# Optimization experiments

Measured on AMD Instinct MI355X. Metric: run time of the kernel, lower is better.

## Reference

```python
import jax, jax.numpy as jnp
import numpy as np

NEG_SLOPE = 0.2  # PyG GATConv default leaky_relu slope
N_NODES, N_EDGES, F_IN, HID = 25000, 200000, 64, 128


def gat_layer(x, src, dst, W, a_src, a_dst, b, heads, ch):
    """PyG-style GATConv (concat=True, eval mode). x:[N,Fin] -> [N,heads*ch]."""
    N = x.shape[0]
    h = (x @ W).reshape(N, heads, ch)                      # [N,H,C]
    al_s = jnp.sum(h * a_src, axis=-1)                     # [N,H]
    al_d = jnp.sum(h * a_dst, axis=-1)                     # [N,H]
    e = jax.nn.leaky_relu(al_s[src] + al_d[dst], NEG_SLOPE)  # [E,H]
    # segment softmax over incoming edges of each dst node (stable)
    e = e - jax.ops.segment_max(e, dst, num_segments=N)[dst]
    ex = jnp.exp(e)
    alpha = ex / jax.ops.segment_sum(ex, dst, num_segments=N)[dst]  # [E,H]
    out = jax.ops.segment_sum(h[src] * alpha[:, :, None], dst, num_segments=N)  # [N,H,C]
    return out.reshape(N, heads * ch) + b


def setup_inputs() -> dict:
    key = jax.random.key(0)
    ks = jax.random.split(key, 24)
    def g(k, shape, fan_in):
        return jax.random.normal(k, shape, dtype=jnp.float32) / np.sqrt(fan_in)
    inp = {
        "x": jax.random.normal(ks[0], (N_NODES, F_IN), dtype=jnp.float32),
        "edge_index": jax.random.randint(ks[1], (2, N_EDGES), 0, N_NODES, dtype=jnp.int64) if jax.config.jax_enable_x64 else jax.random.randint(ks[1], (2, N_EDGES), 0, N_NODES).astype(jnp.int32),
        "liquor_idx": jax.random.randint(ks[2], (4096,), 0, N_NODES),
        "ingredient_idx": jax.random.randint(ks[3], (4096,), 0, N_NODES),
        "W1": g(ks[4], (F_IN, 8 * HID), F_IN), "a_s1": g(ks[5], (8, HID), HID), "a_d1": g(ks[6], (8, HID), HID), "b1": jnp.zeros((8 * HID,), jnp.float32),
        "W2": g(ks[7], (8 * HID, 8 * HID), 8 * HID), "a_s2": g(ks[8], (8, HID), HID), "a_d2": g(ks[9], (8, HID), HID), "b2": jnp.zeros((8 * HID,), jnp.float32),
        "W3": g(ks[10], (8 * HID, HID), 8 * HID), "a_s3": g(ks[11], (1, HID), HID), "a_d3": g(ks[12], (1, HID), HID), "b3": jnp.zeros((HID,), jnp.float32),
        # MLP scorer: 256 -> 128 -> 64 -> 1
        "mw1": g(ks[13], (2 * HID, HID), 2 * HID), "mb1": jnp.zeros((HID,), jnp.float32),
        "mw2": g(ks[14], (HID, HID // 2), HID), "mb2": jnp.zeros((HID // 2,), jnp.float32),
        "mw3": g(ks[15], (HID // 2, 1), HID // 2), "mb3": jnp.zeros((1,), jnp.float32),
    }
    return inp


def reference(x, edge_index, liquor_idx, ingredient_idx,
              W1, a_s1, a_d1, b1, W2, a_s2, a_d2, b2, W3, a_s3, a_d3, b3,
              mw1, mb1, mw2, mb2, mw3, mb3):
    N = x.shape[0]
    loops = jnp.arange(N, dtype=edge_index.dtype)  # GATConv adds self-loops
    src = jnp.concatenate([edge_index[0], loops])
    dst = jnp.concatenate([edge_index[1], loops])
    h = jax.nn.relu(gat_layer(x, src, dst, W1, a_s1, a_d1, b1, 8, HID))
    h = jax.nn.relu(gat_layer(h, src, dst, W2, a_s2, a_d2, b2, 8, HID))
    h = gat_layer(h, src, dst, W3, a_s3, a_d3, b3, 1, HID)
    pair = jnp.concatenate([h[liquor_idx], h[ingredient_idx]], axis=-1)  # [B,256]
    z = jax.nn.relu(pair @ mw1 + mb1)
    z = jax.nn.relu(z @ mw2 + mb2)
    z = z @ mw3 + mb3
    return jax.nn.sigmoid(z).squeeze(-1)
```

## Files before the change

### kernel.cpp

```cpp
#include <hip/hip_runtime.h>
#include <math.h>

#define NEG_SLOPE 0.2f

typedef short short8 __attribute__((ext_vector_type(8)));
typedef float f32x4 __attribute__((ext_vector_type(4)));

__device__ __forceinline__ float lrelu(float x){ return x > 0.f ? x : NEG_SLOPE * x; }

__device__ __forceinline__ unsigned short f2bf(float f){
  union { float f; unsigned u; } v; v.f = f;
  unsigned r = v.u + 0x7fff + ((v.u >> 16) & 1);
  return (unsigned short)(r >> 16);
}
__device__ __forceinline__ float bf2f(unsigned short u){
  union { unsigned u; float f; } v; v.u = ((unsigned)u) << 16; return v.f;
}

__device__ __forceinline__ void gld16(const unsigned short* g, unsigned short* l){
  __builtin_amdgcn_global_load_lds(
      (const __attribute__((address_space(1))) unsigned int*)g,
      (__attribute__((address_space(3))) unsigned int*)l, 16, 0, 0);
}

#define MFMA_BF16 __builtin_amdgcn_mfma_f32_16x16x32_bf16

__global__ void k_count(const int* __restrict__ dst, int* __restrict__ cnt, int E){
  int e = blockIdx.x*blockDim.x + threadIdx.x;
  if (e < E) atomicAdd(&cnt[dst[e]], 1);
}

__global__ void k_blockscan(const int* __restrict__ cnt, int* __restrict__ row,
                            int* __restrict__ aux, int n){
  __shared__ int buf[256];
  int t = threadIdx.x;
  int base = blockIdx.x * 256;
  int v = (base + t < n) ? cnt[base + t] : 0;
  buf[t] = v;
  __syncthreads();
  #pragma unroll
  for (int off = 1; off < 256; off <<= 1){
    int u = (t >= off) ? buf[t - off] : 0;
    __syncthreads();
    buf[t] += u;
    __syncthreads();
  }
  if (base + t < n) row[base + t + 1] = buf[t];
  if (t == 255) aux[blockIdx.x] = buf[255];
  if (blockIdx.x == 0 && t == 0) row[0] = 0;
}

__global__ void k_addoff(const int* __restrict__ aux, int* __restrict__ row, int n){
  __shared__ int sbuf[256];
  int b = blockIdx.x, t = threadIdx.x;
  sbuf[t] = (t < b) ? aux[t] : 0;
  __syncthreads();
  #pragma unroll
  for (int off = 128; off >= 1; off >>= 1){
    if (t < off) sbuf[t] += sbuf[t + off];
    __syncthreads();
  }
  int i = b * 256 + t;
  if (i < n) row[i + 1] += sbuf[0];
}

__global__ void k_scatter(const int* __restrict__ src, const int* __restrict__ dst,
                          const int* __restrict__ row, int* __restrict__ cur,
                          int* __restrict__ csr, int E){
  int e = blockIdx.x*blockDim.x + threadIdx.x;
  if (e < E){
    int d = dst[e];
    int p = atomicAdd(&cur[d], 1);
    csr[row[d] + p] = src[e];
  }
}

__global__ void k_prep(const float* __restrict__ x, unsigned short* __restrict__ xb, int nx, int nxb,
                       const float* __restrict__ W1, unsigned short* __restrict__ Wt1,
                       const float* __restrict__ W2, unsigned short* __restrict__ Wt2,
                       const float* __restrict__ W3, unsigned short* __restrict__ Wt3){
  __shared__ float tile[32][33];
  int b = blockIdx.x, t = threadIdx.x;
  if (b < nxb){
    int i0 = b * 2048 + t * 8;
    if (i0 + 8 <= nx){
      float4 f0 = *reinterpret_cast<const float4*>(x + i0);
      float4 f1 = *reinterpret_cast<const float4*>(x + i0 + 4);
      short8 o;
      o[0]=f2bf(f0.x); o[1]=f2bf(f0.y); o[2]=f2bf(f0.z); o[3]=f2bf(f0.w);
      o[4]=f2bf(f1.x); o[5]=f2bf(f1.y); o[6]=f2bf(f1.z); o[7]=f2bf(f1.w);
      *reinterpret_cast<short8*>(xb + i0) = o;
    } else {
      for (int k = 0; k < 8 && i0 + k < nx; ++k) xb[i0 + k] = f2bf(x[i0 + k]);
    }
    return;
  }
  const float* W; unsigned short* Wt; int K, N, ti;
  if (b < nxb + 64)            { W = W1; Wt = Wt1; K = 64;   N = 1024; ti = b - nxb;
                                 int kb = (ti & 1) * 32, nb = (ti >> 1) * 32;
                                 int tx = t & 31, ty = t >> 5;
                                 #pragma unroll
                                 for (int i = ty; i < 32; i += 8) tile[i][tx] = W[(size_t)(kb+i)*N + nb+tx];
                                 __syncthreads();
                                 #pragma unroll
                                 for (int i = ty; i < 32; i += 8) Wt[(size_t)(nb+i)*K + kb+tx] = f2bf(tile[tx][i]);
                                 return; }
  if (b < nxb + 64 + 1024)     { W = W2; Wt = Wt2; K = 1024; N = 1024; ti = b - nxb - 64; }
  else                         { W = W3; Wt = Wt3; K = 1024; N = 128;  ti = b - nxb - 64 - 1024; }
  int kb = (ti & 31) * 32, nb = (ti >> 5) * 32;
  int tx = t & 31, ty = t >> 5;
  #pragma unroll
  for (int i = ty; i < 32; i += 8) tile[i][tx] = W[(size_t)(kb+i)*N + nb+tx];
  __syncthreads();
  #pragma unroll
  for (int i = ty; i < 32; i += 8) Wt[(size_t)(nb+i)*K + kb+tx] = f2bf(tile[tx][i]);
}

__global__ void k_fold(const float* __restrict__ W1, const float* __restrict__ a_s,
                       const float* __restrict__ a_d, float* __restrict__ ws){
  int k = blockIdx.x, t = threadIdx.x;
  int h = t >> 5, l = t & 31;
  float4 wv = *reinterpret_cast<const float4*>(&W1[(size_t)k * 1024 + h * 128 + l * 4]);
  float4 sv = *reinterpret_cast<const float4*>(&a_s[h * 128 + l * 4]);
  float4 dv = *reinterpret_cast<const float4*>(&a_d[h * 128 + l * 4]);
  float ps = wv.x*sv.x + wv.y*sv.y + wv.z*sv.z + wv.w*sv.w;
  float pd = wv.x*dv.x + wv.y*dv.y + wv.z*dv.z + wv.w*dv.w;
  #pragma unroll
  for (int off = 16; off >= 1; off >>= 1){
    ps += __shfl_xor(ps, off);
    pd += __shfl_xor(pd, off);
  }
  if (l == 0){ ws[k * 16 + h] = ps; ws[k * 16 + 8 + h] = pd; }
}

__global__ void k_logits1(const unsigned short* __restrict__ xb, const float* __restrict__ ws,
                          float* __restrict__ ALS, float* __restrict__ ALD, int N){
  __shared__ unsigned short lx[32 * 64];
  __shared__ float lw[64 * 16];
  int t = threadIdx.x;
  int n0 = blockIdx.x * 32;
  int r = t >> 3, c = (t & 7) * 8;
  if (n0 + r < N)
    *reinterpret_cast<short8*>(&lx[r * 64 + c]) =
      *reinterpret_cast<const short8*>(&xb[(size_t)(n0 + r) * 64 + c]);
  else {
    short8 z = {0,0,0,0,0,0,0,0};
    *reinterpret_cast<short8*>(&lx[r * 64 + c]) = z;
  }
  *reinterpret_cast<float4*>(&lw[t * 4]) = *reinterpret_cast<const float4*>(&ws[t * 4]);
  __syncthreads();
  int nl = t >> 3, h = t & 7;
  if (n0 + nl >= N) return;
  float s = 0.f, d = 0.f;
  #pragma unroll 8
  for (int k = 0; k < 64; ++k){
    float xv = bf2f(lx[nl * 64 + k]);
    s = fmaf(xv, lw[k * 16 + h], s);
    d = fmaf(xv, lw[k * 16 + 8 + h], d);
  }
  ALS[(size_t)(n0 + nl) * 8 + h] = s;
  ALD[(size_t)(n0 + nl) * 8 + h] = d;
}

template<int HEADS>
__global__ void k_sm(const float* __restrict__ ALS, const float* __restrict__ ALD,
                     const int* __restrict__ row, const int* __restrict__ csr,
                     float* __restrict__ alpha, float* __restrict__ alps,
                     float* __restrict__ invl, int N){
  int idx = blockIdx.x * blockDim.x + threadIdx.x;
  int n = idx / HEADS, h = idx - n * HEADS;
  if (n >= N) return;
  float ald = ALD[(size_t)n * HEADS + h];
  float es = lrelu(ALS[(size_t)n * HEADS + h] + ald);
  float m = es;
  int beg = row[n], end = row[n + 1];
  for (int j = beg; j < end; ++j)
    m = fmaxf(m, lrelu(ALS[(size_t)csr[j] * HEADS + h] + ald));
  float ps = __expf(es - m);
  float l = ps;
  for (int j = beg; j < end; ++j){
    float p = __expf(lrelu(ALS[(size_t)csr[j] * HEADS + h] + ald) - m);
    alpha[(size_t)j * HEADS + h] = p;
    l += p;
  }
  alps[(size_t)n * HEADS + h] = ps;
  invl[(size_t)n * HEADS + h] = 1.f / l;
}

__global__ void k_gat_x(const unsigned short* __restrict__ xb, const float* __restrict__ alpha,
                        const float* __restrict__ alps, const float* __restrict__ invl,
                        const int* __restrict__ row, const int* __restrict__ csr,
                        unsigned short* __restrict__ G, int N){
  int t = threadIdx.x;
  int n = blockIdx.x * 4 + (t >> 6);
  if (n >= N) return;
  int lane = t & 63;
  float xv = bf2f(xb[(size_t)n * 64 + lane]);
  float4 s0 = *reinterpret_cast<const float4*>(&alps[(size_t)n * 8]);
  float4 s1 = *reinterpret_cast<const float4*>(&alps[(size_t)n * 8 + 4]);
  float acc[8] = {s0.x*xv, s0.y*xv, s0.z*xv, s0.w*xv, s1.x*xv, s1.y*xv, s1.z*xv, s1.w*xv};
  int beg = row[n], end = row[n + 1];
  for (int j = beg; j < end; ++j){
    int s = csr[j];
    float xs = bf2f(xb[(size_t)s * 64 + lane]);
    float4 a0 = *reinterpret_cast<const float4*>(&alpha[(size_t)j * 8]);
    float4 a1 = *reinterpret_cast<const float4*>(&alpha[(size_t)j * 8 + 4]);
    acc[0] = fmaf(a0.x, xs, acc[0]);
    acc[1] = fmaf(a0.y, xs, acc[1]);
    acc[2] = fmaf(a0.z, xs, acc[2]);
    acc[3] = fmaf(a0.w, xs, acc[3]);
    acc[4] = fmaf(a1.x, xs, acc[4]);
    acc[5] = fmaf(a1.y, xs, acc[5]);
    acc[6] = fmaf(a1.z, xs, acc[6]);
    acc[7] = fmaf(a1.w, xs, acc[7]);
  }
  float4 i0 = *reinterpret_cast<const float4*>(&invl[(size_t)n * 8]);
  float4 i1 = *reinterpret_cast<const float4*>(&invl[(size_t)n * 8 + 4]);
  float iv[8] = {i0.x, i0.y, i0.z, i0.w, i1.x, i1.y, i1.z, i1.w};
  #pragma unroll
  for (int h = 0; h < 8; ++h)
    G[(size_t)n * 512 + h * 64 + lane] = f2bf(acc[h] * iv[h]);
}

__global__ __launch_bounds__(256) void k_gemm_g(
    const unsigned short* __restrict__ G,
    const unsigned short* __restrict__ Bt,
    const float* __restrict__ bias,
    unsigned short* __restrict__ C,
    int M){
  __shared__ unsigned short As[128 * 32];
  __shared__ unsigned short Bs[128 * 32];
  const int nwg = gridDim.x;
  int bid = blockIdx.x;
  int swz = ((nwg & 7) == 0) ? ((bid & 7) * (nwg >> 3) + (bid >> 3)) : bid;
  const int head = swz % 8, byi = swz / 8;
  const int bm = byi * 128, bn = head * 128;
  const int tid  = threadIdx.x;
  const int lane = tid & 63, wave = tid >> 6;
  const int wr = wave >> 1, wc = wave & 1;
  const int lr = lane & 15, lk = lane >> 4;
  const int srow = wave * 16 + (lane >> 2);
  const int skc  = (lane & 3) * 8;
  int ar0 = bm + srow;      if (ar0 >= M) ar0 = M - 1;
  int ar1 = bm + srow + 64; if (ar1 >= M) ar1 = M - 1;
  const unsigned short* ga0 = G + (size_t)ar0 * 512 + head * 64 + skc;
  const unsigned short* ga1 = G + (size_t)ar1 * 512 + head * 64 + skc;
  const unsigned short* gb0 = Bt + (size_t)(bn + srow) * 64 + skc;
  const unsigned short* gb1 = Bt + (size_t)(bn + srow + 64) * 64 + skc;
  f32x4 acc[4][4] = {};
  #pragma unroll
  for (int k0 = 0; k0 < 64; k0 += 32){
    gld16(ga0 + k0, &As[(size_t)wave * 512]);
    gld16(ga1 + k0, &As[(size_t)(wave + 4) * 512]);
    gld16(gb0 + k0, &Bs[(size_t)wave * 512]);
    gld16(gb1 + k0, &Bs[(size_t)(wave + 4) * 512]);
    __syncthreads();
    short8 af[4], bg[4];
    #pragma unroll
    for (int m = 0; m < 4; ++m)
      af[m] = *reinterpret_cast<const short8*>(&As[(wr * 64 + m * 16 + lr) * 32 + lk * 8]);
    #pragma unroll
    for (int n = 0; n < 4; ++n)
      bg[n] = *reinterpret_cast<const short8*>(&Bs[(wc * 64 + n * 16 + lr) * 32 + lk * 8]);
    #pragma unroll
    for (int m = 0; m < 4; ++m)
      #pragma unroll
      for (int n = 0; n < 4; ++n)
        acc[m][n] = MFMA_BF16(af[m], bg[n], acc[m][n], 0, 0, 0);
    __syncthreads();
  }
  float bv[4];
  #pragma unroll
  for (int n = 0; n < 4; ++n) bv[n] = bias[bn + wc * 64 + n * 16 + lr];
  #pragma unroll
  for (int m = 0; m < 4; ++m){
    #pragma unroll
    for (int j = 0; j < 4; ++j){
      int rowi = bm + wr * 64 + m * 16 + lk * 4 + j;
      if (rowi < M){
        #pragma unroll
        for (int n = 0; n < 4; ++n)
          C[(size_t)rowi * 1024 + bn + wc * 64 + n * 16 + lr] = f2bf(fmaxf(acc[m][n][j] + bv[n], 0.f));
      }
    }
  }
}

template<int HEADS>
__global__ __launch_bounds__(256) void k_gemm_fused(
    const unsigned short* __restrict__ A, const unsigned short* __restrict__ Bt,
    unsigned short* __restrict__ C,
    const float* __restrict__ a_s, const float* __restrict__ a_d,
    float* __restrict__ ALS, float* __restrict__ ALD,
    int M, int N, int K, int gxc){
  __shared__ unsigned short SMEM[2 * 128 * 32];
  unsigned short* As = SMEM;
  unsigned short* Bs = SMEM + 128 * 32;
  const int nwg = gridDim.x;
  int bid = blockIdx.x;
  int swz = ((nwg & 7) == 0) ? ((bid & 7) * (nwg >> 3) + (bid >> 3)) : bid;
  const int bxi = swz % gxc, byi = swz / gxc;
  const int bm = byi * 128, bn = bxi * 128;
  const int head = bxi;
  const int tid  = threadIdx.x;
  const int lane = tid & 63, wave = tid >> 6;
  const int wr = wave >> 1, wc = wave & 1;
  const int lr = lane & 15, lk = lane >> 4;
  const int srow = wave * 16 + (lane >> 2);
  const int skc  = (lane & 3) * 8;
  int ar0 = bm + srow;      if (ar0 >= M) ar0 = M - 1;
  int ar1 = bm + srow + 64; if (ar1 >= M) ar1 = M - 1;
  const unsigned short* ga0 = A  + (size_t)ar0 * K + skc;
  const unsigned short* ga1 = A  + (size_t)ar1 * K + skc;
  const unsigned short* gb0 = Bt + (size_t)(bn + srow) * K + skc;
  const unsigned short* gb1 = Bt + (size_t)(bn + srow + 64) * K + skc;
  f32x4 acc[4][4] = {};
  for (int k0 = 0; k0 < K; k0 += 32){
    gld16(ga0 + k0, &As[(size_t)wave * 512]);
    gld16(ga1 + k0, &As[(size_t)(wave + 4) * 512]);
    gld16(gb0 + k0, &Bs[(size_t)wave * 512]);
    gld16(gb1 + k0, &Bs[(size_t)(wave + 4) * 512]);
    __syncthreads();
    short8 af[4], bg[4];
    #pragma unroll
    for (int m = 0; m < 4; ++m)
      af[m] = *reinterpret_cast<const short8*>(&As[(wr * 64 + m * 16 + lr) * 32 + lk * 8]);
    #pragma unroll
    for (int n = 0; n < 4; ++n)
      bg[n] = *reinterpret_cast<const short8*>(&Bs[(wc * 64 + n * 16 + lr) * 32 + lk * 8]);
    #pragma unroll
    for (int m = 0; m < 4; ++m)
      #pragma unroll
      for (int n = 0; n < 4; ++n)
        acc[m][n] = MFMA_BF16(af[m], bg[n], acc[m][n], 0, 0, 0);
    __syncthreads();
  }
  #pragma unroll
  for (int m = 0; m < 4; ++m){
    #pragma unroll
    for (int j = 0; j < 4; ++j){
      int rowi = bm + wr * 64 + m * 16 + lk * 4 + j;
      if (rowi < M){
        #pragma unroll
        for (int n = 0; n < 4; ++n)
          C[(size_t)rowi * N + bn + wc * 64 + n * 16 + lr] = f2bf(acc[m][n][j]);
      }
    }
  }
  float as4[4], ad4[4];
  #pragma unroll
  for (int n = 0; n < 4; ++n){
    as4[n] = a_s[head * 128 + wc * 64 + n * 16 + lr];
    ad4[n] = a_d[head * 128 + wc * 64 + n * 16 + lr];
  }
  float* red = (float*)SMEM;
  #pragma unroll
  for (int m = 0; m < 4; ++m){
    #pragma unroll
    for (int j = 0; j < 4; ++j){
      float ps = 0.f;
      #pragma unroll
      for (int n = 0; n < 4; ++n) ps = fmaf(acc[m][n][j], as4[n], ps);
      red[(wr * 64 + m * 16 + lk * 4 + j) * 32 + wc * 16 + lr] = ps;
    }
  }
  __syncthreads();
  if (tid < 128){
    float s = 0.f;
    #pragma unroll
    for (int i = 0; i < 32; ++i) s += red[tid * 32 + ((i + tid) & 31)];
    int gr = bm + tid;
    if (gr < M) ALS[(size_t)gr * HEADS + head] = s;
  }
  __syncthreads();
  #pragma unroll
  for (int m = 0; m < 4; ++m){
    #pragma unroll
    for (int j = 0; j < 4; ++j){
      float pd = 0.f;
      #pragma unroll
      for (int n = 0; n < 4; ++n) pd = fmaf(acc[m][n][j], ad4[n], pd);
      red[(wr * 64 + m * 16 + lk * 4 + j) * 32 + wc * 16 + lr] = pd;
    }
  }
  __syncthreads();
  if (tid < 128){
    float s = 0.f;
    #pragma unroll
    for (int i = 0; i < 32; ++i) s += red[tid * 32 + ((i + tid) & 31)];
    int gr = bm + tid;
    if (gr < M) ALD[(size_t)gr * HEADS + head] = s;
  }
}

__global__ __launch_bounds__(512, 2) void k_gemm256p8(
    const unsigned short* __restrict__ A,
    const unsigned short* __restrict__ Bt,
    unsigned short* __restrict__ C,
    const float* __restrict__ a_s, const float* __restrict__ a_d,
    float* __restrict__ ALS, float* __restrict__ ALD,
    int M, int N, int K, int gxc){
  __shared__ unsigned short smem[2 * 32768];
  const int nwg = gridDim.x;
  int bid = blockIdx.x;
  int swz = ((nwg & 7) == 0) ? ((bid & 7) * (nwg >> 3) + (bid >> 3)) : bid;
  const int bxi = swz % gxc, byi = swz / gxc;
  const int bm = byi * 256, bn = bxi * 256;
  const int tid = threadIdx.x;
  const int lane = tid & 63, wave = tid >> 6;
  const int wr = wave >> 2, wc = wave & 3;
  const int lr = lane & 15, lk = lane >> 4;
  const int sr = tid >> 3;
  const int scol = ((tid & 7) << 3) ^ ((sr & 7) << 3);
  unsigned offA[4], offB[4];
  #pragma unroll
  for (int u = 0; u < 4; ++u){
    int r = bm + u * 64 + sr; if (r >= M) r = M - 1;
    offA[u] = (unsigned)r * (unsigned)K + scol;
    offB[u] = (unsigned)(bn + u * 64 + sr) * (unsigned)K + scol;
  }
  const int wdst = wave * 512;
  const int NKT = K >> 6;
  const int NIT = NKT >> 1;

  #define STA(T,u) gld16(A  + (size_t)offA[u] + (size_t)(T)*64, &smem[((T)&1)*32768 + (u)*4096 + wdst])
  #define STB(T,u) gld16(Bt + (size_t)offB[u] + (size_t)(T)*64, &smem[((T)&1)*32768 + 16384 + (u)*4096 + wdst])

  #pragma unroll
  for (int u = 0; u < 4; ++u) STA(0, u);
  #pragma unroll
  for (int u = 0; u < 4; ++u) STB(0, u);
  #pragma unroll
  for (int u = 0; u < 4; ++u) STA(1, u);
  asm volatile("s_waitcnt vmcnt(4)" ::: "memory");
  __builtin_amdgcn_s_barrier();

  f32x4 acc[8][4] = {};
  short8 af[4][2], bg[4][2];

  #define RD_A(moff) \
    _Pragma("unroll") \
    for (int m = 0; m < 4; ++m){ \
      int row = wr * 128 + (m + (moff)) * 16 + lr; \
      int rb = row * 64, sw = (row & 7) << 3; \
      af[m][0] = *reinterpret_cast<const short8*>(&sa[rb + ((lk * 8) ^ sw)]); \
      af[m][1] = *reinterpret_cast<const short8*>(&sa[rb + ((32 + lk * 8) ^ sw)]); \
    }
  #define RD_B(n0_, n1_) \
    _Pragma("unroll") \
    for (int n = (n0_); n < (n1_); ++n){ \
      int row = wc * 64 + n * 16 + lr; \
      int rb = row * 64, sw = (row & 7) << 3; \
      bg[n][0] = *reinterpret_cast<const short8*>(&sb[rb + ((lk * 8) ^ sw)]); \
      bg[n][1] = *reinterpret_cast<const short8*>(&sb[rb + ((32 + lk * 8) ^ sw)]); \
    }
  #define SYNC_MFMA_BEG \
    __builtin_amdgcn_s_barrier(); \
    asm volatile("s_waitcnt lgkmcnt(0)" ::: "memory"); \
    __builtin_amdgcn_sched_barrier(0); \
    __builtin_amdgcn_s_setprio(1);
  #define QUAD(mb, nb) \
    _Pragma("unroll") \
    for (int m = 0; m < 4; ++m) \
      _Pragma("unroll") \
      for (int n = 0; n < 2; ++n){ \
        acc[(mb)+m][(nb)+n] = MFMA_BF16(af[m][0], bg[(nb)+n][0], acc[(mb)+m][(nb)+n], 0, 0, 0); \
        acc[(mb)+m][(nb)+n] = MFMA_BF16(af[m][1], bg[(nb)+n][1], acc[(mb)+m][(nb)+n], 0, 0, 0); \
      }
  #define SYNC_MFMA_END \
    __builtin_amdgcn_s_setprio(0); \
    __builtin_amdgcn_s_barrier();

  for (int it = 0; it < NIT; ++it){
    const int T = it << 1;
    {
      const unsigned short* sa = &smem[(T & 1) * 32768];
      const unsigned short* sb = sa + 16384;
      RD_A(0); RD_B(0, 2);
      STB(T + 1, 0); STB(T + 1, 1);
      SYNC_MFMA_BEG; QUAD(0, 0); SYNC_MFMA_END;
      RD_B(2, 4);
      STB(T + 1, 2); STB(T + 1, 3);
      SYNC_MFMA_BEG; QUAD(0, 2); SYNC_MFMA_END;
      RD_A(4);
      if (T + 2 < NKT){ STA(T + 2, 0); STA(T + 2, 2); }
      SYNC_MFMA_BEG; QUAD(4, 0); SYNC_MFMA_END;
      if (T + 2 < NKT){ STA(T + 2, 1); STA(T + 2, 3); }
      __builtin_amdgcn_s_barrier();
      __builtin_amdgcn_s_setprio(1);
      QUAD(4, 2);
      __builtin_amdgcn_s_setprio(0);
      asm volatile("s_waitcnt vmcnt(4)" ::: "memory");
      __builtin_amdgcn_s_barrier();
    }
    {
      const unsigned short* sa = &smem[((T + 1) & 1) * 32768];
      const unsigned short* sb = sa + 16384;
      RD_A(0); RD_B(0, 2);
      if (T + 2 < NKT){ STB(T + 2, 0); STB(T + 2, 1); }
      SYNC_MFMA_BEG; QUAD(0, 0); SYNC_MFMA_END;
      RD_B(2, 4);
      if (T + 2 < NKT){ STB(T + 2, 2); STB(T + 2, 3); }
      SYNC_MFMA_BEG; QUAD(0, 2); SYNC_MFMA_END;
      RD_A(4);
      if (T + 3 < NKT){ STA(T + 3, 0); STA(T + 3, 2); }
      SYNC_MFMA_BEG; QUAD(4, 0); SYNC_MFMA_END;
      if (T + 3 < NKT){ STA(T + 3, 1); STA(T + 3, 3); }
      __builtin_amdgcn_s_barrier();
      __builtin_amdgcn_s_setprio(1);
      QUAD(4, 2);
      __builtin_amdgcn_s_setprio(0);
      asm volatile("s_waitcnt vmcnt(4)" ::: "memory");
      __builtin_amdgcn_s_barrier();
    }
  }

  #pragma unroll
  for (int m = 0; m < 8; ++m){
    #pragma unroll
    for (int j = 0; j < 4; ++j){
      int row = bm + wr * 128 + m * 16 + lk * 4 + j;
      if (row < M){
        #pragma unroll
        for (int n = 0; n < 4; ++n)
          C[(size_t)row * N + bn + wc * 64 + n * 16 + lr] = f2bf(acc[m][n][j]);
      }
    }
  }
  const int hloc = wc >> 1;
  float as4[4], ad4[4];
  #pragma unroll
  for (int n = 0; n < 4; ++n){
    as4[n] = a_s[(bxi * 2 + hloc) * 128 + (wc & 1) * 64 + n * 16 + lr];
    ad4[n] = a_d[(bxi * 2 + hloc) * 128 + (wc & 1) * 64 + n * 16 + lr];
  }
  float2* red = (float2*)smem;
  __syncthreads();
  #pragma unroll
  for (int hh = 0; hh < 2; ++hh){
    if (hloc == hh){
      #pragma unroll
      for (int m = 0; m < 8; ++m){
        #pragma unroll
        for (int j = 0; j < 4; ++j){
          float ps = 0.f, pd = 0.f;
          #pragma unroll
          for (int n = 0; n < 4; ++n){
            ps = fmaf(acc[m][n][j], as4[n], ps);
            pd = fmaf(acc[m][n][j], ad4[n], pd);
          }
          red[(wr * 128 + m * 16 + lk * 4 + j) * 32 + (wc & 1) * 16 + lr] = make_float2(ps, pd);
        }
      }
    }
    __syncthreads();
    if (tid < 256){
      float ss = 0.f, sd = 0.f;
      #pragma unroll
      for (int i = 0; i < 32; ++i){
        float2 v = red[tid * 32 + ((i + tid) & 31)];
        ss += v.x; sd += v.y;
      }
      int gr = bm + tid;
      if (gr < M){
        ALS[(size_t)gr * 8 + bxi * 2 + hh] = ss;
        ALD[(size_t)gr * 8 + bxi * 2 + hh] = sd;
      }
    }
    __syncthreads();
  }
  #undef STA
  #undef STB
  #undef RD_A
  #undef RD_B
  #undef SYNC_MFMA_BEG
  #undef QUAD
  #undef SYNC_MFMA_END
}

__global__ void k_gat2(const unsigned short* __restrict__ hp, const float* __restrict__ alpha,
                       const float* __restrict__ alps, const float* __restrict__ invl,
                       const int* __restrict__ row, const int* __restrict__ csr,
                       const float* __restrict__ bias, unsigned short* __restrict__ outv, int N){
  int n = blockIdx.x;
  int t = threadIdx.x;
  int h = t >> 4;
  int c0 = (t & 15) * 8;
  float sp = alps[(size_t)n * 8 + h];
  const unsigned short* hpn = hp + ((size_t)n * 8 + h) * 128 + c0;
  short8 hv8 = *reinterpret_cast<const short8*>(hpn);
  float accA[8], accB[8] = {};
  #pragma unroll
  for (int v = 0; v < 8; ++v) accA[v] = sp * bf2f((unsigned short)hv8[v]);
  int beg = row[n], end = row[n + 1];
  int j = beg;
  for (; j + 1 < end; j += 2){
    int s0 = csr[j], s1 = csr[j + 1];
    float p0 = alpha[(size_t)j * 8 + h];
    float p1 = alpha[(size_t)(j + 1) * 8 + h];
    short8 v0 = *reinterpret_cast<const short8*>(hp + ((size_t)s0 * 8 + h) * 128 + c0);
    short8 v1 = *reinterpret_cast<const short8*>(hp + ((size_t)s1 * 8 + h) * 128 + c0);
    #pragma unroll
    for (int v = 0; v < 8; ++v){
      accA[v] = fmaf(p0, bf2f((unsigned short)v0[v]), accA[v]);
      accB[v] = fmaf(p1, bf2f((unsigned short)v1[v]), accB[v]);
    }
  }
  if (j < end){
    int s0 = csr[j];
    float p0 = alpha[(size_t)j * 8 + h];
    short8 v0 = *reinterpret_cast<const short8*>(hp + ((size_t)s0 * 8 + h) * 128 + c0);
    #pragma unroll
    for (int v = 0; v < 8; ++v) accA[v] = fmaf(p0, bf2f((unsigned short)v0[v]), accA[v]);
  }
  float inv = invl[(size_t)n * 8 + h];
  size_t ob = ((size_t)n * 8 + h) * 128 + c0;
  #pragma unroll
  for (int v = 0; v < 8; ++v){
    float o = fmaxf((accA[v] + accB[v]) * inv + bias[h * 128 + c0 + v], 0.f);
    outv[ob + v] = f2bf(o);
  }
}

__global__ void k_gat3(const unsigned short* __restrict__ hp, const float* __restrict__ alpha,
                       const float* __restrict__ alps, const float* __restrict__ invl,
                       const int* __restrict__ row, const int* __restrict__ csr,
                       const float* __restrict__ bias,
                       const int* __restrict__ liq, const int* __restrict__ ing,
                       float* __restrict__ out, int NB){
  int b = blockIdx.x;
  int n = (b < NB) ? liq[b] : ing[b - NB];
  int t = threadIdx.x;
  int c0 = t * 2;
  float sp = alps[n];
  ushort2 hv2 = *reinterpret_cast<const ushort2*>(hp + (size_t)n * 128 + c0);
  float a0 = sp * bf2f(hv2.x), a1 = sp * bf2f(hv2.y);
  int beg = row[n], end = row[n + 1];
  for (int j = beg; j < end; ++j){
    int s = csr[j];
    float p = alpha[j];
    ushort2 v = *reinterpret_cast<const ushort2*>(hp + (size_t)s * 128 + c0);
    a0 = fmaf(p, bf2f(v.x), a0);
    a1 = fmaf(p, bf2f(v.y), a1);
  }
  float inv = invl[n];
  out[(size_t)b * 128 + c0]     = a0 * inv + bias[c0];
  out[(size_t)b * 128 + c0 + 1] = a1 * inv + bias[c0 + 1];
}

__global__ void k_mlp(const float* __restrict__ h3,
                      const float* __restrict__ mw1, const float* __restrict__ mb1,
                      const float* __restrict__ mw2, const float* __restrict__ mb2,
                      const float* __restrict__ mw3, const float* __restrict__ mb3,
                      float* __restrict__ out, int B){
  __shared__ float pairv[256];
  __shared__ float z1[128];
  __shared__ float z2[64];
  int r = blockIdx.x;
  int t = threadIdx.x;
  pairv[t]       = h3[(size_t)r * 128 + t];
  pairv[128 + t] = h3[(size_t)(B + r) * 128 + t];
  __syncthreads();
  float a1 = mb1[t];
  for (int k = 0; k < 256; ++k) a1 = fmaf(pairv[k], mw1[k * 128 + t], a1);
  z1[t] = fmaxf(a1, 0.f);
  __syncthreads();
  if (t < 64){
    float a2 = mb2[t];
    for (int k = 0; k < 128; ++k) a2 = fmaf(z1[k], mw2[k * 64 + t], a2);
    z2[t] = fmaxf(a2, 0.f);
  }
  __syncthreads();
  if (t < 64){
    float p = z2[t] * mw3[t];
    #pragma unroll
    for (int off = 32; off >= 1; off >>= 1) p += __shfl_xor(p, off);
    if (t == 0) out[r] = 1.f / (1.f + __expf(-(p + mb3[0])));
  }
}

extern "C" void kernel_launch(void* const* d_in, const int* in_sizes, int n_in,
                              void* d_out, int out_size, void* d_ws, size_t ws_size,
                              hipStream_t stream){
  const float* x   = (const float*)d_in[0];
  const int*   ei  = (const int*)  d_in[1];
  const int*   liq = (const int*)  d_in[2];
  const int*   ing = (const int*)  d_in[3];
  const float* W1  = (const float*)d_in[4];
  const float* as1 = (const float*)d_in[5];
  const float* ad1 = (const float*)d_in[6];
  const float* b1  = (const float*)d_in[7];
  const float* W2  = (const float*)d_in[8];
  const float* as2 = (const float*)d_in[9];
  const float* ad2 = (const float*)d_in[10];
  const float* b2  = (const float*)d_in[11];
  const float* W3  = (const float*)d_in[12];
  const float* as3 = (const float*)d_in[13];
  const float* ad3 = (const float*)d_in[14];
  const float* b3  = (const float*)d_in[15];
  const float* mw1 = (const float*)d_in[16];
  const float* mb1 = (const float*)d_in[17];
  const float* mw2 = (const float*)d_in[18];
  const float* mb2 = (const float*)d_in[19];
  const float* mw3 = (const float*)d_in[20];
  const float* mb3 = (const float*)d_in[21];
  float* out = (float*)d_out;

  const int N = in_sizes[0] / 64;
  const int E = in_sizes[1] / 2;
  const int B = in_sizes[2];
  const int* srcp = ei;
  const int* dstp = ei + E;

  char* w = (char*)d_ws;
  auto alloc = [&](size_t bytes) -> char* {
    char* p = w;
    w += (bytes + 255) & ~(size_t)255;
    return p;
  };
  unsigned short* P    = (unsigned short*)alloc((size_t)N * 1024 * 2);
  unsigned short* Hb   = (unsigned short*)alloc((size_t)N * 1024 * 2);
  float*          H3   = (float*)         alloc((size_t)2 * B * 128 * 4);
  unsigned short* xb   = (unsigned short*)alloc((size_t)N * 64 * 2);
  unsigned short* Wt1  = (unsigned short*)alloc((size_t)1024 * 64 * 2);
  unsigned short* Wt2  = (unsigned short*)alloc((size_t)1024 * 1024 * 2);
  unsigned short* Wt3  = (unsigned short*)alloc((size_t)128 * 1024 * 2);
  float* ALS  = (float*)alloc((size_t)N * 8 * 4);
  float* ALD  = (float*)alloc((size_t)N * 8 * 4);
  float* alpha= (float*)alloc((size_t)E * 8 * 4);
  float* alps = (float*)alloc((size_t)N * 8 * 4);
  float* invl = (float*)alloc((size_t)N * 8 * 4);
  float* ws1  = (float*)alloc((size_t)64 * 16 * 4);
  int*   row  = (int*)  alloc((size_t)(N + 1) * 4);
  int*   cntcur = (int*)alloc((size_t)2 * N * 4);
  int*   cnt  = cntcur;
  int*   cur  = cntcur + N;
  int*   aux  = (int*)  alloc((size_t)256 * 4);
  int*   csr  = (int*)  alloc((size_t)E * 4);
  unsigned short* G = P;
  (void)ws_size; (void)n_in; (void)out_size;

  int nx = N * 64;
  int nxb = (nx + 2047) / 2048;
  k_prep<<<nxb + 64 + 1024 + 128, 256, 0, stream>>>(x, xb, nx, nxb, W1, Wt1, W2, Wt2, W3, Wt3);
  k_fold<<<64, 256, 0, stream>>>(W1, as1, ad1, ws1);

  hipMemsetAsync(cntcur, 0, (size_t)2 * N * 4, stream);
  int eb = (E + 255) / 256;
  int nb = (N + 255) / 256;
  k_count<<<eb, 256, 0, stream>>>(dstp, cnt, E);
  k_blockscan<<<nb, 256, 0, stream>>>(cnt, row, aux, N);
  k_addoff<<<nb, 256, 0, stream>>>(aux, row, N);
  k_scatter<<<eb, 256, 0, stream>>>(srcp, dstp, row, cur, csr, E);

  const int mt  = (N + 127) / 128;
  const int mt2 = (N + 255) / 256;
  const int smb8 = (N * 8 + 255) / 256;
  const int smb1 = (N + 255) / 256;

  k_logits1<<<(N + 31) / 32, 256, 0, stream>>>(xb, ws1, ALS, ALD, N);
  k_sm<8><<<smb8, 256, 0, stream>>>(ALS, ALD, row, csr, alpha, alps, invl, N);
  k_gat_x<<<(N + 3) / 4, 256, 0, stream>>>(xb, alpha, alps, invl, row, csr, G, N);
  k_gemm_g<<<8 * mt, 256, 0, stream>>>(G, Wt1, b1, Hb, N);

  k_gemm256p8<<<4 * mt2, 512, 0, stream>>>(Hb, Wt2, P, as2, ad2, ALS, ALD, N, 1024, 1024, 4);
  k_sm<8><<<smb8, 256, 0, stream>>>(ALS, ALD, row, csr, alpha, alps, invl, N);
  k_gat2<<<N, 128, 0, stream>>>(P, alpha, alps, invl, row, csr, b2, Hb, N);

  k_gemm_fused<1><<<1 * mt, 256, 0, stream>>>(Hb, Wt3, P, as3, ad3, ALS, ALD, N, 128, 1024, 1);
  k_sm<1><<<smb1, 256, 0, stream>>>(ALS, ALD, row, csr, alpha, alps, invl, N);
  k_gat3<<<2 * B, 64, 0, stream>>>(P, alpha, alps, invl, row, csr, b3, liq, ing, H3, B);

  k_mlp<<<B, 128, 0, stream>>>(H3, mw1, mb1, mw2, mb2, mw3, mb3, out, B);
}
```

Baseline: 332.0 us.

## Fuse layer-3 softmax, gather and MLP into one kernel; fold k_fold into k_prep

Merges the weight-fold kernel into the prep kernel as extra blocks, which saves one launch. It also replaces the layer-3 segment-softmax over all nodes, the per-pair gather and the MLP kernel with a single kernel. That kernel computes the softmax only for the queried liquor and ingredient nodes, then runs the MLP. This removes two launches and skips layer-3 softmax work for nodes that are never queried, at the cost of recomputing edge logits twice per queried node.

```diff
diff --git a/kernel.cpp b/kernel.cpp
--- a/kernel.cpp
+++ b/kernel.cpp
@@ -78,7 +78,9 @@
 __global__ void k_prep(const float* __restrict__ x, unsigned short* __restrict__ xb, int nx, int nxb,
                        const float* __restrict__ W1, unsigned short* __restrict__ Wt1,
                        const float* __restrict__ W2, unsigned short* __restrict__ Wt2,
-                       const float* __restrict__ W3, unsigned short* __restrict__ Wt3){
+                       const float* __restrict__ W3, unsigned short* __restrict__ Wt3,
+                       const float* __restrict__ a_s1, const float* __restrict__ a_d1,
+                       float* __restrict__ ws1){
   __shared__ float tile[32][33];
   int b = blockIdx.x, t = threadIdx.x;
   if (b < nxb){
@@ -95,18 +97,35 @@
     }
     return;
   }
+  int bp = b - nxb;
+  if (bp >= 64 + 1024 + 128){
+    int k = bp - (64 + 1024 + 128);
+    int h = t >> 5, lq = t & 31;
+    float4 wv = *reinterpret_cast<const float4*>(&W1[(size_t)k * 1024 + h * 128 + lq * 4]);
+    float4 sv = *reinterpret_cast<const float4*>(&a_s1[h * 128 + lq * 4]);
+    float4 dv = *reinterpret_cast<const float4*>(&a_d1[h * 128 + lq * 4]);
+    float ps = wv.x*sv.x + wv.y*sv.y + wv.z*sv.z + wv.w*sv.w;
+    float pd = wv.x*dv.x + wv.y*dv.y + wv.z*dv.z + wv.w*dv.w;
+    #pragma unroll
+    for (int off = 16; off >= 1; off >>= 1){
+      ps += __shfl_xor(ps, off);
+      pd += __shfl_xor(pd, off);
+    }
+    if (lq == 0){ ws1[k * 16 + h] = ps; ws1[k * 16 + 8 + h] = pd; }
+    return;
+  }
   const float* W; unsigned short* Wt; int K, N, ti;
-  if (b < nxb + 64)            { W = W1; Wt = Wt1; K = 64;   N = 1024; ti = b - nxb;
-                                 int kb = (ti & 1) * 32, nb = (ti >> 1) * 32;
-                                 int tx = t & 31, ty = t >> 5;
-                                 #pragma unroll
-                                 for (int i = ty; i < 32; i += 8) tile[i][tx] = W[(size_t)(kb+i)*N + nb+tx];
-                                 __syncthreads();
-                                 #pragma unroll
-                                 for (int i = ty; i < 32; i += 8) Wt[(size_t)(nb+i)*K + kb+tx] = f2bf(tile[tx][i]);
-                                 return; }
-  if (b < nxb + 64 + 1024)     { W = W2; Wt = Wt2; K = 1024; N = 1024; ti = b - nxb - 64; }
-  else                         { W = W3; Wt = Wt3; K = 1024; N = 128;  ti = b - nxb - 64 - 1024; }
+  if (bp < 64)            { W = W1; Wt = Wt1; K = 64;   N = 1024; ti = bp;
+                            int kb = (ti & 1) * 32, nb = (ti >> 1) * 32;
+                            int tx = t & 31, ty = t >> 5;
+                            #pragma unroll
+                            for (int i = ty; i < 32; i += 8) tile[i][tx] = W[(size_t)(kb+i)*N + nb+tx];
+                            __syncthreads();
+                            #pragma unroll
+                            for (int i = ty; i < 32; i += 8) Wt[(size_t)(nb+i)*K + kb+tx] = f2bf(tile[tx][i]);
+                            return; }
+  if (bp < 64 + 1024)     { W = W2; Wt = Wt2; K = 1024; N = 1024; ti = bp - 64; }
+  else                    { W = W3; Wt = Wt3; K = 1024; N = 128;  ti = bp - 64 - 1024; }
   int kb = (ti & 31) * 32, nb = (ti >> 5) * 32;
   int tx = t & 31, ty = t >> 5;
   #pragma unroll
@@ -114,23 +133,6 @@
   __syncthreads();
   #pragma unroll
   for (int i = ty; i < 32; i += 8) Wt[(size_t)(nb+i)*K + kb+tx] = f2bf(tile[tx][i]);
-}
-
-__global__ void k_fold(const float* __restrict__ W1, const float* __restrict__ a_s,
-                       const float* __restrict__ a_d, float* __restrict__ ws){
-  int k = blockIdx.x, t = threadIdx.x;
-  int h = t >> 5, l = t & 31;
-  float4 wv = *reinterpret_cast<const float4*>(&W1[(size_t)k * 1024 + h * 128 + l * 4]);
-  float4 sv = *reinterpret_cast<const float4*>(&a_s[h * 128 + l * 4]);
-  float4 dv = *reinterpret_cast<const float4*>(&a_d[h * 128 + l * 4]);
-  float ps = wv.x*sv.x + wv.y*sv.y + wv.z*sv.z + wv.w*sv.w;
-  float pd = wv.x*dv.x + wv.y*dv.y + wv.z*dv.z + wv.w*dv.w;
-  #pragma unroll
-  for (int off = 16; off >= 1; off >>= 1){
-    ps += __shfl_xor(ps, off);
-    pd += __shfl_xor(pd, off);
-  }
-  if (l == 0){ ws[k * 16 + h] = ps; ws[k * 16 + 8 + h] = pd; }
 }
 
 __global__ void k_logits1(const unsigned short* __restrict__ xb, const float* __restrict__ ws,
@@ -622,48 +624,49 @@
   }
 }
 
-__global__ void k_gat3(const unsigned short* __restrict__ hp, const float* __restrict__ alpha,
-                       const float* __restrict__ alps, const float* __restrict__ invl,
+__global__ void k_pair(const unsigned short* __restrict__ hp,
+                       const float* __restrict__ al, const float* __restrict__ aldv,
                        const int* __restrict__ row, const int* __restrict__ csr,
                        const float* __restrict__ bias,
                        const int* __restrict__ liq, const int* __restrict__ ing,
-                       float* __restrict__ out, int NB){
-  int b = blockIdx.x;
-  int n = (b < NB) ? liq[b] : ing[b - NB];
-  int t = threadIdx.x;
-  int c0 = t * 2;
-  float sp = alps[n];
-  ushort2 hv2 = *reinterpret_cast<const ushort2*>(hp + (size_t)n * 128 + c0);
-  float a0 = sp * bf2f(hv2.x), a1 = sp * bf2f(hv2.y);
-  int beg = row[n], end = row[n + 1];
-  for (int j = beg; j < end; ++j){
-    int s = csr[j];
-    float p = alpha[j];
-    ushort2 v = *reinterpret_cast<const ushort2*>(hp + (size_t)s * 128 + c0);
-    a0 = fmaf(p, bf2f(v.x), a0);
-    a1 = fmaf(p, bf2f(v.y), a1);
-  }
-  float inv = invl[n];
-  out[(size_t)b * 128 + c0]     = a0 * inv + bias[c0];
-  out[(size_t)b * 128 + c0 + 1] = a1 * inv + bias[c0 + 1];
-}
-
-__global__ void k_mlp(const float* __restrict__ h3,
-                      const float* __restrict__ mw1, const float* __restrict__ mb1,
-                      const float* __restrict__ mw2, const float* __restrict__ mb2,
-                      const float* __restrict__ mw3, const float* __restrict__ mb3,
-                      float* __restrict__ out, int B){
+                       const float* __restrict__ mw1, const float* __restrict__ mb1,
+                       const float* __restrict__ mw2, const float* __restrict__ mb2,
+                       const float* __restrict__ mw3, const float* __restrict__ mb3,
+                       float* __restrict__ out, int B){
   __shared__ float pairv[256];
   __shared__ float z1[128];
   __shared__ float z2[64];
   int r = blockIdx.x;
   int t = threadIdx.x;
-  pairv[t]       = h3[(size_t)r * 128 + t];
-  pairv[128 + t] = h3[(size_t)(B + r) * 128 + t];
-  __syncthreads();
-  float a1 = mb1[t];
-  for (int k = 0; k < 256; ++k) a1 = fmaf(pairv[k], mw1[k * 128 + t], a1);
-  z1[t] = fmaxf(a1, 0.f);
+  int w = t >> 6;
+  int lane = t & 63;
+  int n = w ? ing[r] : liq[r];
+  float ald = aldv[n];
+  float es = lrelu(al[n] + ald);
+  int beg = row[n], end = row[n + 1];
+  float m = es;
+  for (int j = beg; j < end; ++j)
+    m = fmaxf(m, lrelu(al[csr[j]] + ald));
+  float ps = __expf(es - m);
+  float l = ps;
+  int c0 = lane * 2;
+  ushort2 hv = *reinterpret_cast<const ushort2*>(hp + (size_t)n * 128 + c0);
+  float a0 = ps * bf2f(hv.x), a1 = ps * bf2f(hv.y);
+  for (int j = beg; j < end; ++j){
+    int s = csr[j];
+    float p = __expf(lrelu(al[s] + ald) - m);
+    ushort2 v = *reinterpret_cast<const ushort2*>(hp + (size_t)s * 128 + c0);
+    a0 = fmaf(p, bf2f(v.x), a0);
+    a1 = fmaf(p, bf2f(v.y), a1);
+    l += p;
+  }
+  float inv = 1.f / l;
+  pairv[w * 128 + c0]     = a0 * inv + bias[c0];
+  pairv[w * 128 + c0 + 1] = a1 * inv + bias[c0 + 1];
+  __syncthreads();
+  float acc1 = mb1[t];
+  for (int k = 0; k < 256; ++k) acc1 = fmaf(pairv[k], mw1[k * 128 + t], acc1);
+  z1[t] = fmaxf(acc1, 0.f);
   __syncthreads();
   if (t < 64){
     float a2 = mb2[t];
@@ -677,6 +680,7 @@
     for (int off = 32; off >= 1; off >>= 1) p += __shfl_xor(p, off);
     if (t == 0) out[r] = 1.f / (1.f + __expf(-(p + mb3[0])));
   }
+  (void)B;
 }
 
 extern "C" void kernel_launch(void* const* d_in, const int* in_sizes, int n_in,
@@ -720,7 +724,6 @@
   };
   unsigned short* P    = (unsigned short*)alloc((size_t)N * 1024 * 2);
   unsigned short* Hb   = (unsigned short*)alloc((size_t)N * 1024 * 2);
-  float*          H3   = (float*)         alloc((size_t)2 * B * 128 * 4);
   unsigned short* xb   = (unsigned short*)alloc((size_t)N * 64 * 2);
   unsigned short* Wt1  = (unsigned short*)alloc((size_t)1024 * 64 * 2);
   unsigned short* Wt2  = (unsigned short*)alloc((size_t)1024 * 1024 * 2);
@@ -742,8 +745,8 @@
 
   int nx = N * 64;
   int nxb = (nx + 2047) / 2048;
-  k_prep<<<nxb + 64 + 1024 + 128, 256, 0, stream>>>(x, xb, nx, nxb, W1, Wt1, W2, Wt2, W3, Wt3);
-  k_fold<<<64, 256, 0, stream>>>(W1, as1, ad1, ws1);
+  k_prep<<<nxb + 64 + 1024 + 128 + 64, 256, 0, stream>>>(
+      x, xb, nx, nxb, W1, Wt1, W2, Wt2, W3, Wt3, as1, ad1, ws1);
 
   hipMemsetAsync(cntcur, 0, (size_t)2 * N * 4, stream);
   int eb = (E + 255) / 256;
@@ -756,7 +759,6 @@
   const int mt  = (N + 127) / 128;
   const int mt2 = (N + 255) / 256;
   const int smb8 = (N * 8 + 255) / 256;
-  const int smb1 = (N + 255) / 256;
 
   k_logits1<<<(N + 31) / 32, 256, 0, stream>>>(xb, ws1, ALS, ALD, N);
   k_sm<8><<<smb8, 256, 0, stream>>>(ALS, ALD, row, csr, alpha, alps, invl, N);
@@ -768,8 +770,6 @@
   k_gat2<<<N, 128, 0, stream>>>(P, alpha, alps, invl, row, csr, b2, Hb, N);
 
   k_gemm_fused<1><<<1 * mt, 256, 0, stream>>>(Hb, Wt3, P, as3, ad3, ALS, ALD, N, 128, 1024, 1);
-  k_sm<1><<<smb1, 256, 0, stream>>>(ALS, ALD, row, csr, alpha, alps, invl, N);
-  k_gat3<<<2 * B, 64, 0, stream>>>(P, alpha, alps, invl, row, csr, b3, liq, ing, H3, B);
-
-  k_mlp<<<B, 128, 0, stream>>>(H3, mw1, mb1, mw2, mb2, mw3, mb3, out, B);
-}
+  k_pair<<<B, 128, 0, stream>>>(P, ALS, ALD, row, csr, b3, liq, ing,
+                                mw1, mb1, mw2, mb2, mw3, mb3, out, B);
+}
```

Measured after the change: 319.8 us. 1.04x faster.
